# Kernel optimization log

Measured on AMD Instinct MI355X. Metric: run time of the kernel, lower is better.

The kernel has to match this reference:

```python
import jax, jax.numpy as jnp
import numpy as np

NUM_NODE_TYPES = 16
NODE_EMBED = 128
EDGE_EMBED = 64
ATTN_DIMS = [64, 64]
EDGE_DIMS = [32, 32]
HEADS = [4, 4]
N = 50000
E = 500000


def _glorot(key, shape):
    s = jnp.sqrt(2.0 / (shape[0] + shape[1]))
    return jax.random.normal(key, shape, jnp.float32) * s


def setup_inputs() -> dict:
    key = jax.random.key(0)
    ks = jax.random.split(key, 20)
    inp = {}
    inp["node_types"] = jax.random.randint(ks[0], (N,), 0, NUM_NODE_TYPES)
    inp["src"] = jax.random.randint(ks[1], (E,), 0, N)
    inp["dst"] = jax.random.randint(ks[2], (E,), 0, N)
    inp["efeats"] = jax.random.normal(ks[3], (E, EDGE_EMBED), jnp.float32)
    inp["embed_table"] = jax.random.normal(ks[4], (NUM_NODE_TYPES, NODE_EMBED), jnp.float32)
    in_n, in_e = NODE_EMBED, EDGE_EMBED
    k = 5
    for i, (on, oe, h) in enumerate(zip(ATTN_DIMS, EDGE_DIMS, HEADS)):
        inp[f"W_src{i}"] = _glorot(ks[k], (in_n, h * on)); k += 1
        inp[f"b_src{i}"] = jnp.zeros((h * on,), jnp.float32)
        inp[f"W_ni{i}"] = _glorot(ks[k], (in_n, h * oe)); k += 1
        inp[f"W_nj{i}"] = _glorot(ks[k], (in_n, h * oe)); k += 1
        inp[f"W_fij{i}"] = _glorot(ks[k], (in_e, h * oe)); k += 1
        inp[f"attn{i}"] = _glorot(ks[k], (h, oe)); k += 1
        inp[f"bias{i}"] = jnp.zeros((h * oe,), jnp.float32)
        in_n, in_e = h * on, h * oe
    return inp


def _egat_layer(src, dst, nf, ef, W_src, b_src, W_ni, W_nj, W_fij, attn, bias, heads, oe, on):
    # per-edge feature: f_ni(src) + f_nj(dst) + f_fij(edge) + bias
    f_ni = nf @ W_ni                                   # (N, H*oe)
    f_nj = nf @ W_nj                                   # (N, H*oe)
    f_fij = ef @ W_fij                                 # (E, H*oe)
    f_out = f_ni[src] + f_nj[dst] + f_fij + bias       # (E, H*oe)
    f_out = jax.nn.leaky_relu(f_out, 0.01).reshape(-1, heads, oe)  # (E, H, oe)
    e = jnp.einsum('ehd,hd->eh', f_out, attn)          # (E, H) attention logits
    # edge_softmax over incoming edges of each dst node
    m = jax.ops.segment_max(e, dst, num_segments=N)    # (N, H)
    ee = jnp.exp(e - m[dst])
    s = jax.ops.segment_sum(ee, dst, num_segments=N)   # (N, H)
    alpha = ee / s[dst]                                # (E, H)
    h_src = (nf @ W_src + b_src).reshape(-1, heads, on)  # (N, H, on)
    msg = h_src[src] * alpha[:, :, None]               # (E, H, on)
    h_new = jax.ops.segment_sum(msg, dst, num_segments=N)  # (N, H, on)
    return h_new, f_out


def reference(node_types, src, dst, efeats, embed_table,
              W_src0, b_src0, W_ni0, W_nj0, W_fij0, attn0, bias0,
              W_src1, b_src1, W_ni1, W_nj1, W_fij1, attn1, bias1):
    nf = embed_table[node_types]                       # (N, NODE_EMBED)
    ef = efeats
    layers = [
        (W_src0, b_src0, W_ni0, W_nj0, W_fij0, attn0, bias0),
        (W_src1, b_src1, W_ni1, W_nj1, W_fij1, attn1, bias1),
    ]
    for i, p in enumerate(layers):
        h, f = _egat_layer(src, dst, nf, ef, *p, HEADS[i], EDGE_DIMS[i], ATTN_DIMS[i])
        nf = jax.nn.elu(h.reshape(N, -1))              # (N, H*on)
        ef = jax.nn.elu(f.reshape(E, -1))              # (E, H*oe)
    return nf, ef
```

## Files before the change

### kernel.cpp

```cpp
#include <hip/hip_runtime.h>
#include <hip/hip_bf16.h>

#define NN 50000
#define NE 500000

__global__ void k_embed(const int* __restrict__ nt, const float* __restrict__ table,
                        float* __restrict__ nf){
  int i = blockIdx.x * 256 + threadIdx.x;
  if (i >= NN * 128) return;
  nf[i] = table[nt[i >> 7] * 128 + (i & 127)];
}

__global__ void k_zero2(int* __restrict__ cnt, int* __restrict__ cur){
  int i = blockIdx.x * 256 + threadIdx.x;
  if (i < NN){ cnt[i] = 0; cur[i] = 0; }
}

__global__ void k_hist(const int* __restrict__ dst, int* __restrict__ cnt){
  int e = blockIdx.x * 256 + threadIdx.x;
  if (e < NE) atomicAdd(&cnt[dst[e]], 1);
}

__global__ __launch_bounds__(1024) void k_scan(const int* __restrict__ cnt,
                                               int* __restrict__ off){
  __shared__ int ws[16];
  __shared__ int blocktot;
  __shared__ int carry_s;
  int tid = threadIdx.x;
  int lane = tid & 63, wv = tid >> 6;
  if (tid == 0) carry_s = 0;
  for (int base = 0; base < NN; base += 1024){
    int i = base + tid;
    int v = (i < NN) ? cnt[i] : 0;
    int x = v;
    #pragma unroll
    for (int d = 1; d < 64; d <<= 1){
      int t = __shfl_up(x, d, 64);
      if (lane >= d) x += t;
    }
    if (lane == 63) ws[wv] = x;
    __syncthreads();
    if (tid == 0){
      int a = 0;
      #pragma unroll
      for (int k2 = 0; k2 < 16; ++k2){ int t = ws[k2]; ws[k2] = a; a += t; }
      blocktot = a;
    }
    __syncthreads();
    int carry = carry_s;
    if (i < NN) off[i] = carry + ws[wv] + (x - v);
    __syncthreads();
    if (tid == 0) carry_s = carry + blocktot;
    __syncthreads();
  }
  if (tid == 0) off[NN] = carry_s;
}

__global__ void k_scatter(const int* __restrict__ src, const int* __restrict__ dst,
                          const int* __restrict__ off, int* __restrict__ cur,
                          int* __restrict__ rank, int* __restrict__ perm_s){
  int e = blockIdx.x * 256 + threadIdx.x;
  if (e >= NE) return;
  int d = dst[e];
  int pos = off[d] + atomicAdd(&cur[d], 1);
  rank[e] = pos;
  perm_s[pos] = src[e];
}

__global__ __launch_bounds__(256) void k_gemm(
    const float* __restrict__ A, const float* __restrict__ W,
    const float* __restrict__ bias, float* __restrict__ C,
    int M, int K, int Nc){
  __shared__ float As[32][132];
  __shared__ float Ws[32][128];
  int tid = threadIdx.x;
  int row0 = blockIdx.x * 128;
  int col0 = blockIdx.y * 128;
  int tr = (tid >> 4) & 15;
  int tc = tid & 15;

  float acc[8][8];
  #pragma unroll
  for (int i = 0; i < 8; ++i)
    #pragma unroll
    for (int j = 0; j < 8; ++j) acc[i][j] = 0.f;

  for (int k0 = 0; k0 < K; k0 += 32){
    #pragma unroll
    for (int q = 0; q < 4; ++q){
      int idx = tid + q * 256;
      int r  = idx >> 3;
      int kk = (idx & 7) * 4;
      float4 v = make_float4(0.f, 0.f, 0.f, 0.f);
      int gr = row0 + r;
      if (gr < M) v = *reinterpret_cast<const float4*>(A + (size_t)gr * K + k0 + kk);
      As[kk+0][r] = v.x; As[kk+1][r] = v.y; As[kk+2][r] = v.z; As[kk+3][r] = v.w;
    }
    #pragma unroll
    for (int q = 0; q < 4; ++q){
      int idx = tid + q * 256;
      int kk = idx >> 5;
      int cc = (idx & 31) * 4;
      *reinterpret_cast<float4*>(&Ws[kk][cc]) =
          *reinterpret_cast<const float4*>(W + (size_t)(k0 + kk) * Nc + col0 + cc);
    }
    __syncthreads();
    #pragma unroll 8
    for (int kk = 0; kk < 32; ++kk){
      float4 a0 = *reinterpret_cast<const float4*>(&As[kk][tr * 4]);
      float4 a1 = *reinterpret_cast<const float4*>(&As[kk][64 + tr * 4]);
      float4 b0 = *reinterpret_cast<const float4*>(&Ws[kk][tc * 4]);
      float4 b1 = *reinterpret_cast<const float4*>(&Ws[kk][64 + tc * 4]);
      float av[8] = {a0.x, a0.y, a0.z, a0.w, a1.x, a1.y, a1.z, a1.w};
      float bv[8] = {b0.x, b0.y, b0.z, b0.w, b1.x, b1.y, b1.z, b1.w};
      #pragma unroll
      for (int i = 0; i < 8; ++i)
        #pragma unroll
        for (int j = 0; j < 8; ++j)
          acc[i][j] += av[i] * bv[j];
    }
    __syncthreads();
  }

  float4 bia0 = make_float4(0.f, 0.f, 0.f, 0.f), bia1 = bia0;
  if (bias){
    bia0 = *reinterpret_cast<const float4*>(bias + col0 + tc * 4);
    bia1 = *reinterpret_cast<const float4*>(bias + col0 + 64 + tc * 4);
  }
  #pragma unroll
  for (int i = 0; i < 8; ++i){
    int gr = row0 + (i >> 2) * 64 + tr * 4 + (i & 3);
    if (gr < M){
      float4 v0 = make_float4(acc[i][0] + bia0.x, acc[i][1] + bia0.y,
                              acc[i][2] + bia0.z, acc[i][3] + bia0.w);
      float4 v1 = make_float4(acc[i][4] + bia1.x, acc[i][5] + bia1.y,
                              acc[i][6] + bia1.z, acc[i][7] + bia1.w);
      *reinterpret_cast<float4*>(C + (size_t)gr * Nc + col0 + tc * 4) = v0;
      *reinterpret_cast<float4*>(C + (size_t)gr * Nc + col0 + 64 + tc * 4) = v1;
    }
  }
}

__global__ __launch_bounds__(256) void k_gemm_edge(
    const float* __restrict__ A, const float* __restrict__ W,
    const float* __restrict__ f_ni, const float* __restrict__ f_nj,
    const float* __restrict__ bias, const float* __restrict__ attn,
    const int* __restrict__ src, const int* __restrict__ dst,
    const int* __restrict__ rank,
    float* __restrict__ ef_out, float* __restrict__ logits_csr,
    int M, int K){
  __shared__ float As[32][132];
  __shared__ float Ws[32][128];
  int tid = threadIdx.x;
  int row0 = blockIdx.x * 128;
  int tr = (tid >> 4) & 15;
  int tc = tid & 15;

  float acc[8][8];
  #pragma unroll
  for (int i = 0; i < 8; ++i)
    #pragma unroll
    for (int j = 0; j < 8; ++j) acc[i][j] = 0.f;

  for (int k0 = 0; k0 < K; k0 += 32){
    #pragma unroll
    for (int q = 0; q < 4; ++q){
      int idx = tid + q * 256;
      int r  = idx >> 3;
      int kk = (idx & 7) * 4;
      float4 v = make_float4(0.f, 0.f, 0.f, 0.f);
      int gr = row0 + r;
      if (gr < M) v = *reinterpret_cast<const float4*>(A + (size_t)gr * K + k0 + kk);
      As[kk+0][r] = v.x; As[kk+1][r] = v.y; As[kk+2][r] = v.z; As[kk+3][r] = v.w;
    }
    #pragma unroll
    for (int q = 0; q < 4; ++q){
      int idx = tid + q * 256;
      int kk = idx >> 5;
      int cc = (idx & 31) * 4;
      *reinterpret_cast<float4*>(&Ws[kk][cc]) =
          *reinterpret_cast<const float4*>(W + (size_t)(k0 + kk) * 128 + cc);
    }
    __syncthreads();
    #pragma unroll 8
    for (int kk = 0; kk < 32; ++kk){
      float4 a0 = *reinterpret_cast<const float4*>(&As[kk][tr * 4]);
      float4 a1 = *reinterpret_cast<const float4*>(&As[kk][64 + tr * 4]);
      float4 b0 = *reinterpret_cast<const float4*>(&Ws[kk][tc * 4]);
      float4 b1 = *reinterpret_cast<const float4*>(&Ws[kk][64 + tc * 4]);
      float av[8] = {a0.x, a0.y, a0.z, a0.w, a1.x, a1.y, a1.z, a1.w};
      float bv[8] = {b0.x, b0.y, b0.z, b0.w, b1.x, b1.y, b1.z, b1.w};
      #pragma unroll
      for (int i = 0; i < 8; ++i)
        #pragma unroll
        for (int j = 0; j < 8; ++j)
          acc[i][j] += av[i] * bv[j];
    }
    __syncthreads();
  }

  float4 at0 = *reinterpret_cast<const float4*>(attn + tc * 4);
  float4 at1 = *reinterpret_cast<const float4*>(attn + 64 + tc * 4);
  float4 bi0 = *reinterpret_cast<const float4*>(bias + tc * 4);
  float4 bi1 = *reinterpret_cast<const float4*>(bias + 64 + tc * 4);
  #pragma unroll
  for (int i = 0; i < 8; ++i){
    int gr = row0 + (i >> 2) * 64 + tr * 4 + (i & 3);
    if (gr >= M) continue;
    int sN = src[gr], dN = dst[gr];
    const float* ni = f_ni + (size_t)sN * 128;
    const float* nj = f_nj + (size_t)dN * 128;
    float4 n0 = *reinterpret_cast<const float4*>(ni + tc * 4);
    float4 n1 = *reinterpret_cast<const float4*>(ni + 64 + tc * 4);
    float4 m0 = *reinterpret_cast<const float4*>(nj + tc * 4);
    float4 m1 = *reinterpret_cast<const float4*>(nj + 64 + tc * 4);
    float v[8];
    v[0] = acc[i][0] + n0.x + m0.x + bi0.x;
    v[1] = acc[i][1] + n0.y + m0.y + bi0.y;
    v[2] = acc[i][2] + n0.z + m0.z + bi0.z;
    v[3] = acc[i][3] + n0.w + m0.w + bi0.w;
    v[4] = acc[i][4] + n1.x + m1.x + bi1.x;
    v[5] = acc[i][5] + n1.y + m1.y + bi1.y;
    v[6] = acc[i][6] + n1.z + m1.z + bi1.z;
    v[7] = acc[i][7] + n1.w + m1.w + bi1.w;
    #pragma unroll
    for (int j = 0; j < 8; ++j) v[j] = (v[j] >= 0.f) ? v[j] : 0.01f * v[j];
    float4 e0 = make_float4(v[0] > 0.f ? v[0] : expm1f(v[0]),
                            v[1] > 0.f ? v[1] : expm1f(v[1]),
                            v[2] > 0.f ? v[2] : expm1f(v[2]),
                            v[3] > 0.f ? v[3] : expm1f(v[3]));
    float4 e1 = make_float4(v[4] > 0.f ? v[4] : expm1f(v[4]),
                            v[5] > 0.f ? v[5] : expm1f(v[5]),
                            v[6] > 0.f ? v[6] : expm1f(v[6]),
                            v[7] > 0.f ? v[7] : expm1f(v[7]));
    *reinterpret_cast<float4*>(ef_out + (size_t)gr * 128 + tc * 4) = e0;
    *reinterpret_cast<float4*>(ef_out + (size_t)gr * 128 + 64 + tc * 4) = e1;
    float p0 = v[0]*at0.x + v[1]*at0.y + v[2]*at0.z + v[3]*at0.w;
    float p1 = v[4]*at1.x + v[5]*at1.y + v[6]*at1.z + v[7]*at1.w;
    p0 += __shfl_xor(p0, 1, 64); p0 += __shfl_xor(p0, 2, 64); p0 += __shfl_xor(p0, 4, 64);
    p1 += __shfl_xor(p1, 1, 64); p1 += __shfl_xor(p1, 2, 64); p1 += __shfl_xor(p1, 4, 64);
    float q0 = __shfl_xor(p0, 8, 64);
    float q1 = __shfl_xor(p1, 8, 64);
    if (tc == 0){
      int pos = rank[gr];
      *reinterpret_cast<float4*>(logits_csr + (size_t)pos * 4) =
          make_float4(p0, q0, p1, q1);
    }
  }
}

__global__ __launch_bounds__(256) void k_agg_csr(
    const int* __restrict__ off, const int* __restrict__ perm_s,
    const float* __restrict__ logits_csr, const float* __restrict__ h_src,
    float* __restrict__ out){
  int n = blockIdx.x;
  int c = threadIdx.x;
  int h = c >> 6;
  int beg = off[n], end = off[n + 1];
  float m = -INFINITY;
  for (int j = beg; j < end; ++j)
    m = fmaxf(m, logits_csr[(size_t)j * 4 + h]);
  float acc = 0.f, ssum = 0.f;
  for (int j = beg; j < end; ++j){
    float ee = expf(logits_csr[(size_t)j * 4 + h] - m);
    ssum += ee;
    acc += ee * h_src[(size_t)perm_s[j] * 256 + c];
  }
  float r = (end > beg) ? acc / ssum : 0.f;
  out[(size_t)n * 256 + c] = (r > 0.f) ? r : expm1f(r);
}

static void run_layer(const float* nf, int in_n, const float* ef, int in_e,
                      const float* Wsrc, const float* bsrc, const float* Wni,
                      const float* Wnj, const float* Wfij, const float* attn,
                      const float* bias, const int* src, const int* dst,
                      const int* off, const int* rank, const int* perm_s,
                      float* f_ni, float* f_nj, float* h_src, float* logits,
                      float* nf_out, float* ef_out, hipStream_t stream){
  dim3 gN((NN + 127) / 128, 1);
  dim3 gN2((NN + 127) / 128, 2);
  k_gemm<<<gN,  256, 0, stream>>>(nf, Wni, nullptr, f_ni, NN, in_n, 128);
  k_gemm<<<gN,  256, 0, stream>>>(nf, Wnj, nullptr, f_nj, NN, in_n, 128);
  k_gemm<<<gN2, 256, 0, stream>>>(nf, Wsrc, bsrc, h_src, NN, in_n, 256);
  k_gemm_edge<<<(NE + 127) / 128, 256, 0, stream>>>(
      ef, Wfij, f_ni, f_nj, bias, attn, src, dst, rank, ef_out, logits, NE, in_e);
  k_agg_csr<<<NN, 256, 0, stream>>>(off, perm_s, logits, h_src, nf_out);
}

extern "C" void kernel_launch(void* const* d_in, const int* in_sizes, int n_in,
                              void* d_out, int out_size, void* d_ws, size_t ws_size,
                              hipStream_t stream){
  const int*   node_types = (const int*)d_in[0];
  const int*   src        = (const int*)d_in[1];
  const int*   dst        = (const int*)d_in[2];
  const float* efeats     = (const float*)d_in[3];
  const float* table      = (const float*)d_in[4];
  const float* W_src0 = (const float*)d_in[5];
  const float* b_src0 = (const float*)d_in[6];
  const float* W_ni0  = (const float*)d_in[7];
  const float* W_nj0  = (const float*)d_in[8];
  const float* W_fij0 = (const float*)d_in[9];
  const float* attn0  = (const float*)d_in[10];
  const float* bias0  = (const float*)d_in[11];
  const float* W_src1 = (const float*)d_in[12];
  const float* b_src1 = (const float*)d_in[13];
  const float* W_ni1  = (const float*)d_in[14];
  const float* W_nj1  = (const float*)d_in[15];
  const float* W_fij1 = (const float*)d_in[16];
  const float* attn1  = (const float*)d_in[17];
  const float* bias1  = (const float*)d_in[18];

  char* w = (char*)d_ws;
  auto alloc = [&](size_t bytes){ void* p = (void*)w; w += (bytes + 255) & ~(size_t)255; return p; };
  float* nf_buf = (float*)alloc((size_t)NN * 256 * 4);
  float* f_ni   = (float*)alloc((size_t)NN * 128 * 4);
  float* f_nj   = (float*)alloc((size_t)NN * 128 * 4);
  float* h_src  = (float*)alloc((size_t)NN * 256 * 4);
  float* logits = (float*)alloc((size_t)NE * 4 * 4);
  int*   cnt    = (int*)  alloc((size_t)NN * 4);
  int*   cur    = (int*)  alloc((size_t)NN * 4);
  int*   off    = (int*)  alloc((size_t)(NN + 1) * 4);
  int*   rank   = (int*)  alloc((size_t)NE * 4);
  int*   perm_s = (int*)  alloc((size_t)NE * 4);

  float* out_nf = (float*)d_out;
  float* out_ef = out_nf + (size_t)NN * 256;

  k_zero2<<<(NN + 255)/256, 256, 0, stream>>>(cnt, cur);
  k_hist<<<(NE + 255)/256, 256, 0, stream>>>(dst, cnt);
  k_scan<<<1, 1024, 0, stream>>>(cnt, off);
  k_scatter<<<(NE + 255)/256, 256, 0, stream>>>(src, dst, off, cur, rank, perm_s);

  k_embed<<<(NN*128)/256, 256, 0, stream>>>(node_types, table, nf_buf);

  run_layer(nf_buf, 128, efeats, 64,
            W_src0, b_src0, W_ni0, W_nj0, W_fij0, attn0, bias0,
            src, dst, off, rank, perm_s,
            f_ni, f_nj, h_src, logits, nf_buf, out_ef, stream);

  run_layer(nf_buf, 256, out_ef, 128,
            W_src1, b_src1, W_ni1, W_nj1, W_fij1, attn1, bias1,
            src, dst, off, rank, perm_s,
            f_ni, f_nj, h_src, logits, out_nf, out_ef, stream);
}
```

Before: 1.614 ms.

## Prefetch GEMM tiles into registers, shrink node GEMM tile, unroll aggregation loop

Both the node GEMM and the edge GEMM now load the next K-slice of A and W into registers while the current slice is being computed, so global-load latency overlaps the FMA work. The node GEMM is templated on row-tile size and launched with 64-row tiles, giving more blocks and lower register use per thread. The CSR aggregation loop is unrolled by four with independent gathers and uses the fast __expf. Register prefetching raises register pressure, and __expf slightly changes numerics.

```diff
diff --git a/kernel.cpp b/kernel.cpp
--- a/kernel.cpp
+++ b/kernel.cpp
@@ -67,54 +67,83 @@
   perm_s[pos] = src[e];
 }
 
-__global__ __launch_bounds__(256) void k_gemm(
+template<int BM>
+__global__ __launch_bounds__(256) void k_gemm_t(
     const float* __restrict__ A, const float* __restrict__ W,
     const float* __restrict__ bias, float* __restrict__ C,
     int M, int K, int Nc){
-  __shared__ float As[32][132];
+  constexpr int RM = BM / 16;
+  constexpr int AQ = BM / 32;
+  __shared__ float As[32][BM + 4];
   __shared__ float Ws[32][128];
   int tid = threadIdx.x;
-  int row0 = blockIdx.x * 128;
+  int row0 = blockIdx.x * BM;
   int col0 = blockIdx.y * 128;
   int tr = (tid >> 4) & 15;
   int tc = tid & 15;
-
-  float acc[8][8];
-  #pragma unroll
-  for (int i = 0; i < 8; ++i)
+  int wk0 = tid >> 5;
+  int wcc = (tid & 31) * 4;
+
+  float4 pa[AQ], pw[4];
+  #pragma unroll
+  for (int q = 0; q < AQ; ++q) pa[q] = make_float4(0.f,0.f,0.f,0.f);
+
+  float acc[RM][8];
+  #pragma unroll
+  for (int i = 0; i < RM; ++i)
     #pragma unroll
     for (int j = 0; j < 8; ++j) acc[i][j] = 0.f;
 
+  #pragma unroll
+  for (int q = 0; q < AQ; ++q){
+    int idx = tid + q * 256;
+    int gr = row0 + (idx >> 3);
+    if (gr < M) pa[q] = *reinterpret_cast<const float4*>(A + (size_t)gr * K + ((idx & 7) * 4));
+  }
+  #pragma unroll
+  for (int q = 0; q < 4; ++q)
+    pw[q] = *reinterpret_cast<const float4*>(W + (size_t)(wk0 + q * 8) * Nc + col0 + wcc);
+
   for (int k0 = 0; k0 < K; k0 += 32){
     #pragma unroll
-    for (int q = 0; q < 4; ++q){
+    for (int q = 0; q < AQ; ++q){
       int idx = tid + q * 256;
-      int r  = idx >> 3;
-      int kk = (idx & 7) * 4;
-      float4 v = make_float4(0.f, 0.f, 0.f, 0.f);
-      int gr = row0 + r;
-      if (gr < M) v = *reinterpret_cast<const float4*>(A + (size_t)gr * K + k0 + kk);
-      As[kk+0][r] = v.x; As[kk+1][r] = v.y; As[kk+2][r] = v.z; As[kk+3][r] = v.w;
-    }
-    #pragma unroll
-    for (int q = 0; q < 4; ++q){
-      int idx = tid + q * 256;
-      int kk = idx >> 5;
-      int cc = (idx & 31) * 4;
-      *reinterpret_cast<float4*>(&Ws[kk][cc]) =
-          *reinterpret_cast<const float4*>(W + (size_t)(k0 + kk) * Nc + col0 + cc);
-    }
-    __syncthreads();
+      int r = idx >> 3, kk = (idx & 7) * 4;
+      As[kk+0][r] = pa[q].x; As[kk+1][r] = pa[q].y;
+      As[kk+2][r] = pa[q].z; As[kk+3][r] = pa[q].w;
+    }
+    #pragma unroll
+    for (int q = 0; q < 4; ++q)
+      *reinterpret_cast<float4*>(&Ws[wk0 + q * 8][wcc]) = pw[q];
+    __syncthreads();
+    if (k0 + 32 < K){
+      int kn = k0 + 32;
+      #pragma unroll
+      for (int q = 0; q < AQ; ++q){
+        int idx = tid + q * 256;
+        int gr = row0 + (idx >> 3);
+        pa[q] = make_float4(0.f,0.f,0.f,0.f);
+        if (gr < M) pa[q] = *reinterpret_cast<const float4*>(A + (size_t)gr * K + kn + ((idx & 7) * 4));
+      }
+      #pragma unroll
+      for (int q = 0; q < 4; ++q)
+        pw[q] = *reinterpret_cast<const float4*>(W + (size_t)(kn + wk0 + q * 8) * Nc + col0 + wcc);
+    }
     #pragma unroll 8
     for (int kk = 0; kk < 32; ++kk){
-      float4 a0 = *reinterpret_cast<const float4*>(&As[kk][tr * 4]);
-      float4 a1 = *reinterpret_cast<const float4*>(&As[kk][64 + tr * 4]);
+      float bv[8];
       float4 b0 = *reinterpret_cast<const float4*>(&Ws[kk][tc * 4]);
       float4 b1 = *reinterpret_cast<const float4*>(&Ws[kk][64 + tc * 4]);
-      float av[8] = {a0.x, a0.y, a0.z, a0.w, a1.x, a1.y, a1.z, a1.w};
-      float bv[8] = {b0.x, b0.y, b0.z, b0.w, b1.x, b1.y, b1.z, b1.w};
-      #pragma unroll
-      for (int i = 0; i < 8; ++i)
+      bv[0]=b0.x; bv[1]=b0.y; bv[2]=b0.z; bv[3]=b0.w;
+      bv[4]=b1.x; bv[5]=b1.y; bv[6]=b1.z; bv[7]=b1.w;
+      float av[RM];
+      #pragma unroll
+      for (int g = 0; g < RM / 4; ++g){
+        float4 a = *reinterpret_cast<const float4*>(&As[kk][g * (BM >> 1) + tr * 4]);
+        av[g*4+0]=a.x; av[g*4+1]=a.y; av[g*4+2]=a.z; av[g*4+3]=a.w;
+      }
+      #pragma unroll
+      for (int i = 0; i < RM; ++i)
         #pragma unroll
         for (int j = 0; j < 8; ++j)
           acc[i][j] += av[i] * bv[j];
@@ -128,8 +157,8 @@
     bia1 = *reinterpret_cast<const float4*>(bias + col0 + 64 + tc * 4);
   }
   #pragma unroll
-  for (int i = 0; i < 8; ++i){
-    int gr = row0 + (i >> 2) * 64 + tr * 4 + (i & 3);
+  for (int i = 0; i < RM; ++i){
+    int gr = row0 + (i >> 2) * (BM >> 1) + tr * 4 + (i & 3);
     if (gr < M){
       float4 v0 = make_float4(acc[i][0] + bia0.x, acc[i][1] + bia0.y,
                               acc[i][2] + bia0.z, acc[i][3] + bia0.w);
@@ -155,41 +184,66 @@
   int row0 = blockIdx.x * 128;
   int tr = (tid >> 4) & 15;
   int tc = tid & 15;
+  int wk0 = tid >> 5;
+  int wcc = (tid & 31) * 4;
+
+  float4 pa[4], pw[4];
+  #pragma unroll
+  for (int q = 0; q < 4; ++q) pa[q] = make_float4(0.f,0.f,0.f,0.f);
 
   float acc[8][8];
   #pragma unroll
   for (int i = 0; i < 8; ++i)
     #pragma unroll
     for (int j = 0; j < 8; ++j) acc[i][j] = 0.f;
+
+  #pragma unroll
+  for (int q = 0; q < 4; ++q){
+    int idx = tid + q * 256;
+    int gr = row0 + (idx >> 3);
+    if (gr < M) pa[q] = *reinterpret_cast<const float4*>(A + (size_t)gr * K + ((idx & 7) * 4));
+  }
+  #pragma unroll
+  for (int q = 0; q < 4; ++q)
+    pw[q] = *reinterpret_cast<const float4*>(W + (size_t)(wk0 + q * 8) * 128 + wcc);
 
   for (int k0 = 0; k0 < K; k0 += 32){
     #pragma unroll
     for (int q = 0; q < 4; ++q){
       int idx = tid + q * 256;
-      int r  = idx >> 3;
-      int kk = (idx & 7) * 4;
-      float4 v = make_float4(0.f, 0.f, 0.f, 0.f);
-      int gr = row0 + r;
-      if (gr < M) v = *reinterpret_cast<const float4*>(A + (size_t)gr * K + k0 + kk);
-      As[kk+0][r] = v.x; As[kk+1][r] = v.y; As[kk+2][r] = v.z; As[kk+3][r] = v.w;
-    }
-    #pragma unroll
-    for (int q = 0; q < 4; ++q){
-      int idx = tid + q * 256;
-      int kk = idx >> 5;
-      int cc = (idx & 31) * 4;
-      *reinterpret_cast<float4*>(&Ws[kk][cc]) =
-          *reinterpret_cast<const float4*>(W + (size_t)(k0 + kk) * 128 + cc);
-    }
-    __syncthreads();
+      int r = idx >> 3, kk = (idx & 7) * 4;
+      As[kk+0][r] = pa[q].x; As[kk+1][r] = pa[q].y;
+      As[kk+2][r] = pa[q].z; As[kk+3][r] = pa[q].w;
+    }
+    #pragma unroll
+    for (int q = 0; q < 4; ++q)
+      *reinterpret_cast<float4*>(&Ws[wk0 + q * 8][wcc]) = pw[q];
+    __syncthreads();
+    if (k0 + 32 < K){
+      int kn = k0 + 32;
+      #pragma unroll
+      for (int q = 0; q < 4; ++q){
+        int idx = tid + q * 256;
+        int gr = row0 + (idx >> 3);
+        pa[q] = make_float4(0.f,0.f,0.f,0.f);
+        if (gr < M) pa[q] = *reinterpret_cast<const float4*>(A + (size_t)gr * K + kn + ((idx & 7) * 4));
+      }
+      #pragma unroll
+      for (int q = 0; q < 4; ++q)
+        pw[q] = *reinterpret_cast<const float4*>(W + (size_t)(kn + wk0 + q * 8) * 128 + wcc);
+    }
     #pragma unroll 8
     for (int kk = 0; kk < 32; ++kk){
+      float bv[8];
+      float4 b0 = *reinterpret_cast<const float4*>(&Ws[kk][tc * 4]);
+      float4 b1 = *reinterpret_cast<const float4*>(&Ws[kk][64 + tc * 4]);
+      bv[0]=b0.x; bv[1]=b0.y; bv[2]=b0.z; bv[3]=b0.w;
+      bv[4]=b1.x; bv[5]=b1.y; bv[6]=b1.z; bv[7]=b1.w;
+      float av[8];
       float4 a0 = *reinterpret_cast<const float4*>(&As[kk][tr * 4]);
       float4 a1 = *reinterpret_cast<const float4*>(&As[kk][64 + tr * 4]);
-      float4 b0 = *reinterpret_cast<const float4*>(&Ws[kk][tc * 4]);
-      float4 b1 = *reinterpret_cast<const float4*>(&Ws[kk][64 + tc * 4]);
-      float av[8] = {a0.x, a0.y, a0.z, a0.w, a1.x, a1.y, a1.z, a1.w};
-      float bv[8] = {b0.x, b0.y, b0.z, b0.w, b1.x, b1.y, b1.z, b1.w};
+      av[0]=a0.x; av[1]=a0.y; av[2]=a0.z; av[3]=a0.w;
+      av[4]=a1.x; av[5]=a1.y; av[6]=a1.z; av[7]=a1.w;
       #pragma unroll
       for (int i = 0; i < 8; ++i)
         #pragma unroll
@@ -261,8 +315,24 @@
   for (int j = beg; j < end; ++j)
     m = fmaxf(m, logits_csr[(size_t)j * 4 + h]);
   float acc = 0.f, ssum = 0.f;
-  for (int j = beg; j < end; ++j){
-    float ee = expf(logits_csr[(size_t)j * 4 + h] - m);
+  int j = beg;
+  for (; j + 4 <= end; j += 4){
+    int s0 = perm_s[j], s1 = perm_s[j+1], s2 = perm_s[j+2], s3 = perm_s[j+3];
+    float l0 = logits_csr[(size_t)j * 4 + h];
+    float l1 = logits_csr[(size_t)(j+1) * 4 + h];
+    float l2 = logits_csr[(size_t)(j+2) * 4 + h];
+    float l3 = logits_csr[(size_t)(j+3) * 4 + h];
+    float g0 = h_src[(size_t)s0 * 256 + c];
+    float g1 = h_src[(size_t)s1 * 256 + c];
+    float g2 = h_src[(size_t)s2 * 256 + c];
+    float g3 = h_src[(size_t)s3 * 256 + c];
+    float e0 = __expf(l0 - m), e1 = __expf(l1 - m);
+    float e2 = __expf(l2 - m), e3 = __expf(l3 - m);
+    ssum += (e0 + e1) + (e2 + e3);
+    acc += e0 * g0 + e1 * g1 + e2 * g2 + e3 * g3;
+  }
+  for (; j < end; ++j){
+    float ee = __expf(logits_csr[(size_t)j * 4 + h] - m);
     ssum += ee;
     acc += ee * h_src[(size_t)perm_s[j] * 256 + c];
   }
@@ -277,11 +347,11 @@
                       const int* off, const int* rank, const int* perm_s,
                       float* f_ni, float* f_nj, float* h_src, float* logits,
                       float* nf_out, float* ef_out, hipStream_t stream){
-  dim3 gN((NN + 127) / 128, 1);
-  dim3 gN2((NN + 127) / 128, 2);
-  k_gemm<<<gN,  256, 0, stream>>>(nf, Wni, nullptr, f_ni, NN, in_n, 128);
-  k_gemm<<<gN,  256, 0, stream>>>(nf, Wnj, nullptr, f_nj, NN, in_n, 128);
-  k_gemm<<<gN2, 256, 0, stream>>>(nf, Wsrc, bsrc, h_src, NN, in_n, 256);
+  dim3 gN((NN + 63) / 64, 1);
+  dim3 gN2((NN + 63) / 64, 2);
+  k_gemm_t<64><<<gN,  256, 0, stream>>>(nf, Wni, nullptr, f_ni, NN, in_n, 128);
+  k_gemm_t<64><<<gN,  256, 0, stream>>>(nf, Wnj, nullptr, f_nj, NN, in_n, 128);
+  k_gemm_t<64><<<gN2, 256, 0, stream>>>(nf, Wsrc, bsrc, h_src, NN, in_n, 256);
   k_gemm_edge<<<(NE + 127) / 128, 256, 0, stream>>>(
       ef, Wfij, f_ni, f_nj, bias, attn, src, dst, rank, ef_out, logits, NE, in_e);
   k_agg_csr<<<NN, 256, 0, stream>>>(off, perm_s, logits, h_src, nf_out);
```

Result: no change. 1.644 ms (+1.9%).
